# Kernel optimization log

Hardware: AMD Instinct MI355X
Metric: run time of the kernel (lower is better)

## Reference

```python
import jax, jax.numpy as jnp
import numpy as np

B, S, E, H = 4, 2048, 1024, 16
D = E // H  # head_dim = 64


def setup_inputs() -> dict:
    key = jax.random.key(0)
    ks = jax.random.split(key, 5)
    return {
        "hidden_states": jax.random.normal(ks[0], (B, S, E), dtype=jnp.float32),
        "c_attn_w": jax.random.normal(ks[1], (E, 3 * E), dtype=jnp.float32) * 0.02,
        "c_attn_b": jax.random.normal(ks[2], (3 * E,), dtype=jnp.float32) * 0.02,
        "c_proj_w": jax.random.normal(ks[3], (E, E), dtype=jnp.float32) * 0.02,
        "c_proj_b": jax.random.normal(ks[4], (E,), dtype=jnp.float32) * 0.02,
    }


def reference(hidden_states, c_attn_w, c_attn_b, c_proj_w, c_proj_b):
    b, s, e = hidden_states.shape
    # Conv1D c_attn: y = x @ W + b  -> qkv [b, s, 3E]
    qkv = hidden_states @ c_attn_w + c_attn_b
    q, k, v = jnp.split(qkv, 3, axis=-1)
    # split heads -> [b, H, s, D]
    def split_heads(t):
        return t.reshape(b, s, H, D).transpose(0, 2, 1, 3)
    q, k, v = split_heads(q), split_heads(k), split_heads(v)
    # QK^T scaled by sqrt(head_dim)
    scores = jnp.einsum("bhqd,bhkd->bhqk", q, k) / jnp.sqrt(
        jnp.asarray(D, dtype=q.dtype)
    )
    # causal mask (tril), masked positions get dtype min
    causal = jnp.tril(jnp.ones((s, s), dtype=bool))[None, None]
    mask_value = jnp.finfo(scores.dtype).min
    scores = jnp.where(causal, scores, mask_value)
    attn = jax.nn.softmax(scores, axis=-1)
    # attend to values, merge heads
    out = jnp.einsum("bhqk,bhkd->bhqd", attn, v)
    out = out.transpose(0, 2, 1, 3).reshape(b, s, e)
    # Conv1D c_proj
    return out @ c_proj_w + c_proj_b
```

## Files before the change

### kernel.cpp

```cpp
#include <hip/hip_runtime.h>
#include <hip/hip_bf16.h>
#include <cstdint>
#include <cstddef>

#define BB 4
#define SS 2048
#define EE 1024
#define HH 16
#define DD 64

typedef __attribute__((ext_vector_type(8))) short bf16x8;
typedef __attribute__((ext_vector_type(4))) float f32x4;

__device__ __forceinline__ short f2bf(float f) {
    union { float f; uint32_t u; } x; x.f = f;
    uint32_t r = (x.u + 0x7fffu + ((x.u >> 16) & 1u)) >> 16;
    return (short)r;
}
__device__ __forceinline__ short f2bf_fast(float f) {
    union { float f; uint32_t u; } x; x.f = f;
    return (short)((x.u + 0x8000u) >> 16);
}

__device__ __forceinline__ void gload16(const void* g, void* l) {
    __builtin_amdgcn_global_load_lds(
        (__attribute__((address_space(1))) uint32_t*)(uintptr_t)g,
        (__attribute__((address_space(3))) uint32_t*)(uint32_t)(uintptr_t)l,
        16, 0, 0);
}

#define WAIT_BARRIER(N)                                          \
    asm volatile("s_waitcnt vmcnt(" #N ")" ::: "memory");        \
    __builtin_amdgcn_s_barrier();                                \
    __builtin_amdgcn_sched_barrier(0);

template<int CTRL>
__device__ __forceinline__ float dppmove(float v) {
    return __int_as_float(__builtin_amdgcn_update_dpp(
        0, __float_as_int(v), CTRL, 0xf, 0xf, true));
}
#define ROW_REDUCE(vals, OP)                                             \
    _Pragma("unroll") for (int _r = 0; _r < 4; ++_r) {                   \
        vals[_r] = OP(vals[_r], dppmove<0xB1>(vals[_r]));                \
        vals[_r] = OP(vals[_r], dppmove<0x4E>(vals[_r]));                \
        vals[_r] = OP(vals[_r], dppmove<0x124>(vals[_r]));               \
        vals[_r] = OP(vals[_r], dppmove<0x128>(vals[_r]));               \
    }
__device__ __forceinline__ float opmax(float a, float b) { return fmaxf(a, b); }
__device__ __forceinline__ float opsum(float a, float b) { return a + b; }

__global__ void cast_kernel(const float* __restrict__ in, short* __restrict__ out, int n4) {
    int stride = gridDim.x * blockDim.x;
    for (int i = blockIdx.x * blockDim.x + threadIdx.x; i < n4; i += stride) {
        float4 v = reinterpret_cast<const float4*>(in)[i];
        short4 o;
        o.x = f2bf(v.x); o.y = f2bf(v.y); o.z = f2bf(v.z); o.w = f2bf(v.w);
        reinterpret_cast<short4*>(out)[i] = o;
    }
}

__global__ void transpose_cast_kernel(const float* __restrict__ in, short* __restrict__ out,
                                      int ncols, int nrows) {
    __shared__ float ts[32][33];
    const int t = threadIdx.x;
    const int r = t >> 3, c4 = (t & 7) * 4;
    const int n0 = blockIdx.x * 32, k0 = blockIdx.y * 32;
    float4 v = *reinterpret_cast<const float4*>(&in[(size_t)(k0 + r) * ncols + n0 + c4]);
    ts[c4 + 0][r] = v.x; ts[c4 + 1][r] = v.y; ts[c4 + 2][r] = v.z; ts[c4 + 3][r] = v.w;
    __syncthreads();
    short4 ov;
    ov.x = f2bf(ts[r][c4 + 0]); ov.y = f2bf(ts[r][c4 + 1]);
    ov.z = f2bf(ts[r][c4 + 2]); ov.w = f2bf(ts[r][c4 + 3]);
    *reinterpret_cast<short4*>(&out[(size_t)(n0 + r) * nrows + k0 + c4]) = ov;
}

template<int MODE>
__global__ __launch_bounds__(256, 2)
void gemm128(const short* __restrict__ A, const short* __restrict__ Bt,
             const float* __restrict__ bias,
             short* __restrict__ Qo, short* __restrict__ Ko, short* __restrict__ Vo,
             float* __restrict__ Co)
{
    __shared__ short As[3][4096];
    __shared__ short Bs[3][4096];
    const int tid  = threadIdx.x;
    const int lane = tid & 63, wid = tid >> 6;
    const int wr = wid >> 1, wc = wid & 1;
    const int l15 = lane & 15, lhi = lane >> 4;
    const int m0 = blockIdx.y * 128, n0 = blockIdx.x * 128;
    const int sr   = lane >> 2;
    const int scol = 8 * ((lane & 3) ^ ((lane >> 3) & 3));
    const int rdx  = (lhi ^ ((l15 >> 1) & 3)) << 4;

    f32x4 acc[4][4] = {};

#define G_STAGE(tt, bufi)                                                        \
    {                                                                            \
        const int kk = (tt) * 32;                                                \
        _Pragma("unroll")                                                        \
        for (int p = 0; p < 2; ++p) {                                            \
            const int c = wid * 2 + p;                                           \
            gload16(&A [(size_t)(m0 + c * 16 + sr) * EE + kk + scol],            \
                    (char*)&As[bufi][0] + c * 1024);                             \
            gload16(&Bt[(size_t)(n0 + c * 16 + sr) * EE + kk + scol],            \
                    (char*)&Bs[bufi][0] + c * 1024);                             \
        }                                                                        \
    }

    G_STAGE(0, 0)
    G_STAGE(1, 1)
    WAIT_BARRIER(4)

    for (int kt = 0; kt < 32; ++kt) {
        const int cur = kt % 3;
        if (kt + 2 < 32) { const int nb = (kt + 2) % 3; G_STAGE(kt + 2, nb) }

        bf16x8 af[4], bfr[4];
        #pragma unroll
        for (int mm = 0; mm < 4; ++mm)
            af[mm] = *reinterpret_cast<const bf16x8*>(
                (const char*)&As[cur][0] + (wr * 64 + mm * 16 + l15) * 64 + rdx);
        #pragma unroll
        for (int nn = 0; nn < 4; ++nn)
            bfr[nn] = *reinterpret_cast<const bf16x8*>(
                (const char*)&Bs[cur][0] + (wc * 64 + nn * 16 + l15) * 64 + rdx);
        #pragma unroll
        for (int mm = 0; mm < 4; ++mm)
            #pragma unroll
            for (int nn = 0; nn < 4; ++nn)
                acc[mm][nn] = __builtin_amdgcn_mfma_f32_16x16x32_bf16(af[mm], bfr[nn], acc[mm][nn], 0, 0, 0);

        if (kt < 30)       { WAIT_BARRIER(4) }
        else if (kt == 30) { WAIT_BARRIER(0) }
    }
#undef G_STAGE

    if (MODE == 0) {
        const int part = n0 >> 10;
        #pragma unroll
        for (int mm = 0; mm < 4; ++mm) {
            #pragma unroll
            for (int nn = 0; nn < 4; ++nn) {
                const int gcol = n0 + wc * 64 + nn * 16 + l15;
                const float bv = bias[gcol];
                const int e = gcol & 1023;
                const int h = e >> 6, d = e & 63;
                const int grow0 = m0 + wr * 64 + mm * 16 + lhi * 4;
                const int bidx = grow0 >> 11;
                const int s0 = grow0 & 2047;
                const int bh = bidx * HH + h;
                if (part == 2) {
                    short4 pk;
                    pk.x = f2bf(acc[mm][nn][0] + bv);
                    pk.y = f2bf(acc[mm][nn][1] + bv);
                    pk.z = f2bf(acc[mm][nn][2] + bv);
                    pk.w = f2bf(acc[mm][nn][3] + bv);
                    *reinterpret_cast<short4*>(&Vo[((size_t)bh * DD + d) * SS + s0]) = pk;
                } else if (part == 0) {
                    #pragma unroll
                    for (int r = 0; r < 4; ++r)
                        Qo[((size_t)bh * SS + s0 + r) * DD + d] = f2bf((acc[mm][nn][r] + bv) * 0.18033688f);
                } else {
                    #pragma unroll
                    for (int r = 0; r < 4; ++r)
                        Ko[((size_t)bh * SS + s0 + r) * DD + d] = f2bf(acc[mm][nn][r] + bv);
                }
            }
        }
    } else {
        #pragma unroll
        for (int mm = 0; mm < 4; ++mm) {
            #pragma unroll
            for (int nn = 0; nn < 4; ++nn) {
                const int gcol = n0 + wc * 64 + nn * 16 + l15;
                const float bv = bias[gcol];
                #pragma unroll
                for (int r = 0; r < 4; ++r) {
                    const int grow = m0 + wr * 64 + mm * 16 + lhi * 4 + r;
                    Co[(size_t)grow * EE + gcol] = acc[mm][nn][r] + bv;
                }
            }
        }
    }
}

__global__ __launch_bounds__(512, 2)
void attn_kernel(const short* __restrict__ Q, const short* __restrict__ K,
                 const short* __restrict__ Vt, short* __restrict__ CTX)
{
    __shared__ short Ks[4096];
    __shared__ short Vs[2][4096];
    __shared__ short Ps[8][1024];
    const int tid  = threadIdx.x;
    const int lane = tid & 63, wid = tid >> 6;
    const int l15 = lane & 15, lhi = lane >> 4;
    const int bid  = blockIdx.x;
    const int bh   = (bid & 7) * 8 + ((bid >> 3) & 7);
    const int pair = bid >> 6;
    const int b = bh >> 4, h = bh & 15;
    const size_t base = (size_t)bh * (SS * DD);
    const short* VtBase = Vt + (size_t)bh * (DD * SS);
    char* const pw = (char*)&Ps[wid][0];

    const int srow = lane >> 3;
    const int scol = 8 * ((lane & 7) ^ srow);

    for (int phase = 0; phase < 2; ++phase) {
        const int t = phase ? (15 - pair) : pair;
        const int q0 = t * 128;
        const int qbase = q0 + wid * 16;
        const int nkt = 2 * t + 2;

        bf16x8 qa[2];
        qa[0] = *reinterpret_cast<const bf16x8*>(&Q[base + (size_t)(qbase + l15) * DD + lhi * 8]);
        qa[1] = *reinterpret_cast<const bf16x8*>(&Q[base + (size_t)(qbase + l15) * DD + 32 + lhi * 8]);

        f32x4 o[4] = {};
        float lrow[4] = {0.f, 0.f, 0.f, 0.f};

        gload16(&K     [base + (size_t)(wid * 8 + srow) * DD + scol], (char*)Ks + wid * 1024);
        gload16(&VtBase[(size_t)(wid * 8 + srow) * SS + scol],        (char*)&Vs[0][0] + wid * 1024);
        __syncthreads();

        for (int kt = 0; kt < nkt; ++kt) {
            const int cur = kt & 1;
            const int k0 = kt * 64;

            f32x4 sc[4];
            #pragma unroll
            for (int n = 0; n < 4; ++n) {
                const int row = n * 16 + l15;
                f32x4 cacc = {};
                #pragma unroll
                for (int ks = 0; ks < 2; ++ks) {
                    const int byteoff = (ks * 64 + lhi * 16) ^ ((l15 & 7) << 4);
                    bf16x8 kb = *reinterpret_cast<const bf16x8*>((const char*)Ks + row * 128 + byteoff);
                    cacc = __builtin_amdgcn_mfma_f32_16x16x32_bf16(qa[ks], kb, cacc, 0, 0, 0);
                }
                sc[n] = cacc;
            }

            __syncthreads();

            if (kt + 1 < nkt) {
                const int k1 = k0 + 64;
                gload16(&K     [base + (size_t)(k1 + wid * 8 + srow) * DD + scol], (char*)Ks + wid * 1024);
                gload16(&VtBase[(size_t)(wid * 8 + srow) * SS + k1 + scol], (char*)&Vs[cur ^ 1][0] + wid * 1024);
            }

            if (k0 + 63 > qbase) {
                #pragma unroll
                for (int n = 0; n < 4; ++n) {
                    const int col = k0 + n * 16 + l15;
                    #pragma unroll
                    for (int r = 0; r < 4; ++r) {
                        const int qrow = qbase + lhi * 4 + r;
                        if (col > qrow) sc[n][r] = -1e30f;
                    }
                }
            }
            #pragma unroll
            for (int n = 0; n < 4; ++n)
                #pragma unroll
                for (int r = 0; r < 4; ++r) sc[n][r] = __builtin_amdgcn_exp2f(sc[n][r]);
            #pragma unroll
            for (int n = 0; n < 4; ++n)
                #pragma unroll
                for (int r = 0; r < 4; ++r) {
                    const int q = lhi * 4 + r;
                    const int cb = (n * 32 + l15 * 2) ^ ((q & 7) << 4);
                    *reinterpret_cast<short*>(pw + q * 128 + cb) = f2bf_fast(sc[n][r]);
                }
            bf16x8 pa[2];
            #pragma unroll
            for (int ks = 0; ks < 2; ++ks)
                pa[ks] = *reinterpret_cast<const bf16x8*>(
                    pw + l15 * 128 + ((ks * 64 + lhi * 16) ^ ((l15 & 7) << 4)));
            #pragma unroll
            for (int dg = 0; dg < 4; ++dg) {
                const int row = dg * 16 + l15;
                #pragma unroll
                for (int ks = 0; ks < 2; ++ks) {
                    const int byteoff = (ks * 64 + lhi * 16) ^ ((l15 & 7) << 4);
                    bf16x8 vb = *reinterpret_cast<const bf16x8*>((const char*)&Vs[cur][0] + row * 128 + byteoff);
                    o[dg] = __builtin_amdgcn_mfma_f32_16x16x32_bf16(pa[ks], vb, o[dg], 0, 0, 0);
                }
            }
            float tsum[4];
            #pragma unroll
            for (int r = 0; r < 4; ++r)
                tsum[r] = (sc[0][r] + sc[1][r]) + (sc[2][r] + sc[3][r]);
            ROW_REDUCE(tsum, opsum)
            #pragma unroll
            for (int r = 0; r < 4; ++r) lrow[r] += tsum[r];

            __syncthreads();
        }

        #pragma unroll
        for (int dg = 0; dg < 4; ++dg)
            #pragma unroll
            for (int r = 0; r < 4; ++r) {
                int s = qbase + lhi * 4 + r;
                float val = o[dg][r] / lrow[r];
                CTX[(size_t)(b * SS + s) * EE + h * DD + dg * 16 + l15] = f2bf(val);
            }
    }
}

extern "C" void kernel_launch(void* const* d_in, const int* in_sizes, int n_in,
                              void* d_out, int out_size, void* d_ws, size_t ws_size,
                              hipStream_t stream) {
    const float* hs     = (const float*)d_in[0];
    const float* attn_w = (const float*)d_in[1];
    const float* attn_b = (const float*)d_in[2];
    const float* proj_w = (const float*)d_in[3];
    const float* proj_b = (const float*)d_in[4];
    float* out = (float*)d_out;

    char* ws = (char*)d_ws;
    short* Xb    = (short*)(ws + 0);
    short* WqkvT = (short*)(ws + 16777216);
    short* WprojT= (short*)(ws + 23068672);
    short* Qb    = (short*)(ws + 25165824);
    short* Kb    = (short*)(ws + 41943040);
    short* Vb    = (short*)(ws + 58720256);
    short* CTX   = Xb;

    cast_kernel<<<dim3(2048), dim3(256), 0, stream>>>(hs, Xb, (BB * SS * EE) / 4);
    transpose_cast_kernel<<<dim3(3 * EE / 32, EE / 32), dim3(256), 0, stream>>>(attn_w, WqkvT, 3 * EE, EE);
    transpose_cast_kernel<<<dim3(EE / 32, EE / 32), dim3(256), 0, stream>>>(proj_w, WprojT, EE, EE);

    gemm128<0><<<dim3(3 * EE / 128, BB * SS / 128), dim3(256), 0, stream>>>(
        Xb, WqkvT, attn_b, Qb, Kb, Vb, nullptr);

    attn_kernel<<<dim3(512), dim3(512), 0, stream>>>(Qb, Kb, Vb, CTX);

    gemm128<1><<<dim3(EE / 128, BB * SS / 128), dim3(256), 0, stream>>>(
        CTX, WprojT, proj_b, nullptr, nullptr, nullptr, out);
}
```

Before: 172.9 us.

## Double-buffer K tile in attention and merge the prep casts into one kernel

The attention loop now keeps two K tiles in LDS, alternating between them. This lets it drop the barrier that separated the QK^T reads from the prefetch of the next K tile, which overwrote the same buffer. The input cast and the two weight transpose-casts are folded into one launch that dispatches on block index, saving two kernel launches. The cost is an extra 8 KB of LDS per attention block, and correctness now depends on later barriers in the loop ordering reuse of the other K buffer.

```diff
diff --git a/kernel.cpp b/kernel.cpp
--- a/kernel.cpp
+++ b/kernel.cpp
@@ -49,29 +49,37 @@
 __device__ __forceinline__ float opmax(float a, float b) { return fmaxf(a, b); }
 __device__ __forceinline__ float opsum(float a, float b) { return a + b; }
 
-__global__ void cast_kernel(const float* __restrict__ in, short* __restrict__ out, int n4) {
-    int stride = gridDim.x * blockDim.x;
-    for (int i = blockIdx.x * blockDim.x + threadIdx.x; i < n4; i += stride) {
-        float4 v = reinterpret_cast<const float4*>(in)[i];
-        short4 o;
-        o.x = f2bf(v.x); o.y = f2bf(v.y); o.z = f2bf(v.z); o.w = f2bf(v.w);
-        reinterpret_cast<short4*>(out)[i] = o;
-    }
-}
-
-__global__ void transpose_cast_kernel(const float* __restrict__ in, short* __restrict__ out,
-                                      int ncols, int nrows) {
+__global__ void prep_kernel(const float* __restrict__ hs, short* __restrict__ Xb,
+                            const float* __restrict__ attn_w, short* __restrict__ WqkvT,
+                            const float* __restrict__ proj_w, short* __restrict__ WprojT)
+{
     __shared__ float ts[32][33];
+    int bid = blockIdx.x;
     const int t = threadIdx.x;
+    if (bid < 2048) {
+        const int n4 = (BB * SS * EE) / 4;
+        const int stride = 2048 * 256;
+        for (int i = bid * 256 + t; i < n4; i += stride) {
+            float4 v = reinterpret_cast<const float4*>(hs)[i];
+            short4 o;
+            o.x = f2bf(v.x); o.y = f2bf(v.y); o.z = f2bf(v.z); o.w = f2bf(v.w);
+            reinterpret_cast<short4*>(Xb)[i] = o;
+        }
+        return;
+    }
+    bid -= 2048;
+    const float* in; short* out; int ncols, bx, by;
+    if (bid < 3072) { in = attn_w; out = WqkvT; ncols = 3 * EE; bx = bid % 96; by = bid / 96; }
+    else { bid -= 3072; in = proj_w; out = WprojT; ncols = EE; bx = bid % 32; by = bid / 32; }
     const int r = t >> 3, c4 = (t & 7) * 4;
-    const int n0 = blockIdx.x * 32, k0 = blockIdx.y * 32;
+    const int n0 = bx * 32, k0 = by * 32;
     float4 v = *reinterpret_cast<const float4*>(&in[(size_t)(k0 + r) * ncols + n0 + c4]);
     ts[c4 + 0][r] = v.x; ts[c4 + 1][r] = v.y; ts[c4 + 2][r] = v.z; ts[c4 + 3][r] = v.w;
     __syncthreads();
     short4 ov;
     ov.x = f2bf(ts[r][c4 + 0]); ov.y = f2bf(ts[r][c4 + 1]);
     ov.z = f2bf(ts[r][c4 + 2]); ov.w = f2bf(ts[r][c4 + 3]);
-    *reinterpret_cast<short4*>(&out[(size_t)(n0 + r) * nrows + k0 + c4]) = ov;
+    *reinterpret_cast<short4*>(&out[(size_t)(n0 + r) * EE + k0 + c4]) = ov;
 }
 
 template<int MODE>
@@ -188,7 +196,7 @@
 void attn_kernel(const short* __restrict__ Q, const short* __restrict__ K,
                  const short* __restrict__ Vt, short* __restrict__ CTX)
 {
-    __shared__ short Ks[4096];
+    __shared__ short Ks[2][4096];
     __shared__ short Vs[2][4096];
     __shared__ short Ps[8][1024];
     const int tid  = threadIdx.x;
@@ -218,7 +226,7 @@
         f32x4 o[4] = {};
         float lrow[4] = {0.f, 0.f, 0.f, 0.f};
 
-        gload16(&K     [base + (size_t)(wid * 8 + srow) * DD + scol], (char*)Ks + wid * 1024);
+        gload16(&K     [base + (size_t)(wid * 8 + srow) * DD + scol], (char*)&Ks[0][0] + wid * 1024);
         gload16(&VtBase[(size_t)(wid * 8 + srow) * SS + scol],        (char*)&Vs[0][0] + wid * 1024);
         __syncthreads();
 
@@ -234,18 +242,18 @@
                 #pragma unroll
                 for (int ks = 0; ks < 2; ++ks) {
                     const int byteoff = (ks * 64 + lhi * 16) ^ ((l15 & 7) << 4);
-                    bf16x8 kb = *reinterpret_cast<const bf16x8*>((const char*)Ks + row * 128 + byteoff);
+                    bf16x8 kb = *reinterpret_cast<const bf16x8*>((const char*)&Ks[cur][0] + row * 128 + byteoff);
                     cacc = __builtin_amdgcn_mfma_f32_16x16x32_bf16(qa[ks], kb, cacc, 0, 0, 0);
                 }
                 sc[n] = cacc;
             }
-
-            __syncthreads();
 
             if (kt + 1 < nkt) {
                 const int k1 = k0 + 64;
-                gload16(&K     [base + (size_t)(k1 + wid * 8 + srow) * DD + scol], (char*)Ks + wid * 1024);
-                gload16(&VtBase[(size_t)(wid * 8 + srow) * SS + k1 + scol], (char*)&Vs[cur ^ 1][0] + wid * 1024);
+                gload16(&K     [base + (size_t)(k1 + wid * 8 + srow) * DD + scol],
+                        (char*)&Ks[cur ^ 1][0] + wid * 1024);
+                gload16(&VtBase[(size_t)(wid * 8 + srow) * SS + k1 + scol],
+                        (char*)&Vs[cur ^ 1][0] + wid * 1024);
             }
 
             if (k0 + 63 > qbase) {
@@ -327,9 +335,8 @@
     short* Vb    = (short*)(ws + 58720256);
     short* CTX   = Xb;
 
-    cast_kernel<<<dim3(2048), dim3(256), 0, stream>>>(hs, Xb, (BB * SS * EE) / 4);
-    transpose_cast_kernel<<<dim3(3 * EE / 32, EE / 32), dim3(256), 0, stream>>>(attn_w, WqkvT, 3 * EE, EE);
-    transpose_cast_kernel<<<dim3(EE / 32, EE / 32), dim3(256), 0, stream>>>(proj_w, WprojT, EE, EE);
+    prep_kernel<<<dim3(2048 + 3072 + 1024), dim3(256), 0, stream>>>(
+        hs, Xb, attn_w, WqkvT, proj_w, WprojT);
 
     gemm128<0><<<dim3(3 * EE / 128, BB * SS / 128), dim3(256), 0, stream>>>(
         Xb, WqkvT, attn_b, Qb, Kb, Vb, nullptr);
```

Measured after the change: 169.3 us. -2.1%, faster.
